# Performance work log

Measured on AMD Instinct MI355X. Metric: run time of the kernel, lower is better.

Reference implementation:

```python
import jax, jax.numpy as jnp
import numpy as np

K = 16
NUM_RBF = 32
MAX_DIST = 24.0
OUT_DIM = 256
_SPACING = MAX_DIST / (NUM_RBF - 1)
GAMMA = 1.0 / (_SPACING * _SPACING + 1e-08)
CENTERS = jnp.linspace(0.0, MAX_DIST, NUM_RBF)


def setup_inputs() -> dict:
    key = jax.random.key(0)
    k1, k2, k3 = jax.random.split(key, 3)
    B, M = 64, 1024
    # scale coords so pairwise distances span roughly [0, MAX_DIST]
    ligand_coords = jax.random.normal(k1, (B, M, 3), dtype=jnp.float32) * 8.0
    ligand_mask = jax.random.randint(k2, (B, M), 0, 2) > 0
    proj_w = jax.random.normal(k3, (OUT_DIM, K * NUM_RBF), dtype=jnp.float32) * 0.05
    return {"ligand_coords": ligand_coords, "ligand_mask": ligand_mask, "proj_w": proj_w}


def reference(ligand_coords, ligand_mask, proj_w):
    B, M, _ = ligand_coords.shape
    x = ligand_coords.astype(jnp.float32)
    # pairwise euclidean distances via the gram trick (avoids [B,M,M,3])
    sq = jnp.sum(x * x, axis=-1)                      # [B, M]
    gram = jnp.einsum('bid,bjd->bij', x, x)           # [B, M, M]
    d2 = sq[:, :, None] + sq[:, None, :] - 2.0 * gram
    dists = jnp.sqrt(jnp.maximum(d2, 1e-12))          # [B, M, M]
    eye = jnp.eye(M, dtype=bool)[None]
    valid_pair = ligand_mask[:, :, None] & ligand_mask[:, None, :]
    invalid = eye | ~valid_pair
    dists = jnp.where(invalid, jnp.inf, dists)
    # k smallest distances per atom
    neg_topk, _ = jax.lax.top_k(-dists, K)            # [B, M, K]
    topk = -neg_topk
    d_padded = jnp.where(jnp.isfinite(topk), topk, MAX_DIST)
    # RBF embed
    diff = d_padded[..., None] - CENTERS              # [B, M, K, NUM_RBF]
    rbf = jnp.exp(-GAMMA * diff * diff)
    rbf_flat = rbf.reshape(B, M, K * NUM_RBF)
    out = jnp.einsum('bmf,of->bmo', rbf_flat, proj_w)
    return out * ligand_mask[..., None].astype(out.dtype)
```

## Files before the change

kernel.cpp:

```cpp
#include <hip/hip_runtime.h>
#include <hip/hip_bf16.h>
#include <math.h>

#define MDIM 1024
#define QTOT 65536
#define KTOP 16
#define ODIM 256
#define FDIM 512

typedef float f32x4 __attribute__((ext_vector_type(4)));
typedef short s16x8 __attribute__((ext_vector_type(8)));
typedef unsigned u32x4 __attribute__((ext_vector_type(4)));

#if __has_builtin(__builtin_amdgcn_exp2f)
#define EXP2(x) __builtin_amdgcn_exp2f(x)
#else
#define EXP2(x) exp2f(x)
#endif

#define VMIN(a,b)    ({float r_; asm("v_min_f32 %0,%1,%2":"=v"(r_):"v"(a),"v"(b)); r_;})
#define VMAX(a,b)    ({float r_; asm("v_max_f32 %0,%1,%2":"=v"(r_):"v"(a),"v"(b)); r_;})

__device__ __forceinline__ int read_mask(const void* m, int i, bool is8) {
  return is8 ? (int)((const unsigned char*)m)[i] : ((const int*)m)[i];
}

__device__ __forceinline__ unsigned pack2(float lo, float hi) {
  __hip_bfloat162 h = __float22bfloat162_rn(make_float2(lo, hi));
  unsigned u;
  __builtin_memcpy(&u, &h, sizeof(u));
  return u;
}

__global__ __launch_bounds__(256) void wconv_kernel(
    const float* __restrict__ W, u32x4* __restrict__ Wb)
{
  int slot = blockIdx.x * 256 + threadIdx.x;
  int cg = slot >> 10;
  int rem = slot & 1023;
  int s = rem >> 6, l = rem & 63;
  int col = cg * 16 + (l & 15);
  int kk = s * 32 + (l >> 4) * 8;
  const float4* p = (const float4*)(W + (size_t)col * FDIM + kk);
  float4 a = p[0], b = p[1];
  u32x4 u0;
  u0[0] = pack2(a.x, a.y); u0[1] = pack2(a.z, a.w);
  u0[2] = pack2(b.x, b.y); u0[3] = pack2(b.z, b.w);
  Wb[(size_t)(cg * 16 + s) * 64 + l] = u0;
}

constexpr double SPd = 24.0 / 31.0;
constexpr double SP2d = SPd * SPd;
constexpr float ALPHA = (float)(-(SP2d / (SP2d + 1e-8)) * 1.4426950408889634);
constexpr float INV_SP = (float)(1.0 / SPd);

__device__ __forceinline__ void gen_cell(u32x4* Ab, int rf, int rowlo, int s, float d0) {
  float d = (d0 < 0.f) ? 1.0e9f : d0;
  float u = d * INV_SP;
  float C1 = (-2.0f * ALPHA) * u;
  float C0 = ALPHA * u * u;
  #pragma unroll
  for (int c8 = 0; c8 < 4; ++c8) {
    u32x4 ch;
    #pragma unroll
    for (int q = 0; q < 4; ++q) {
      const int j0 = c8 * 8 + q * 2;
      float e0 = EXP2(fmaf(C1, (float)j0,       C0) + ALPHA * (float)(j0 * j0));
      float e1 = EXP2(fmaf(C1, (float)(j0 + 1), C0) + ALPHA * (float)((j0 + 1) * (j0 + 1)));
      ch[q] = pack2(e0, e1);
    }
    Ab[rf * 1040 + s * 65 + c8 * 16 + rowlo] = ch;
  }
}

__global__ __launch_bounds__(512, 4) void fused_kernel(
    const float* __restrict__ coords, const void* __restrict__ mask,
    const u32x4* __restrict__ Wb, float* __restrict__ out)
{
  __shared__ __align__(16) char raw[66560];
  __shared__ float dvals[64][17];
  __shared__ int s_cnt;
  __shared__ int s_is8;

  float4* pts = (float4*)raw;
  short* posof = (short*)(raw + 16384);
  u32x4* Ab = (u32x4*)raw;

  const int tid = threadIdx.x;
  const int lane = tid & 63;
  const int wv = tid >> 6;
  const int bid = blockIdx.x;
  const int batch = bid >> 4;
  const int qchunk = bid & 15;

  if (tid == 0) { s_cnt = 0; s_is8 = 0; }
  __syncthreads();
  {
    unsigned w = ((const unsigned*)mask)[tid & 255];
    if (w > 1u) atomicOr(&s_is8, 1);
  }
  __syncthreads();
  const bool is8 = (s_is8 != 0);

  const float* cb = coords + (size_t)batch * MDIM * 3;
  const int mbase = batch * MDIM;

  #pragma unroll
  for (int r = 0; r < 2; ++r) {
    int a = r * 512 + tid;
    int v = read_mask(mask, mbase + a, is8);
    float x = cb[a*3+0], y = cb[a*3+1], z = cb[a*3+2];
    float S = fmaf(z, z, fmaf(y, y, x * x));
    unsigned long long bal = __ballot(v != 0);
    int base = 0;
    if (lane == 0) base = atomicAdd(&s_cnt, __popcll(bal));
    base = __shfl(base, 0);
    int pos = base + __popcll(bal & ((1ull << lane) - 1ull));
    if (v) {
      float4 p; p.x = x; p.y = y; p.z = z; p.w = S;
      pts[pos] = p;
    }
    posof[a] = (short)(v ? pos : -1);
  }
  __syncthreads();
  const int cnt = s_cnt;
  const int cntP = (cnt + 63) & ~63;
  for (int i = cnt + tid; i < cntP; i += 512) {
    float4 p; p.x = 0.f; p.y = 0.f; p.z = 0.f; p.w = 3.0e38f;
    pts[i] = p;
  }
  __syncthreads();

  const int qi = lane & 7;
  const int part = lane >> 3;
  const int qlo = wv * 8 + qi;
  const int qlocal = qchunk * 64 + qlo;
  const float qx = cb[qlocal*3+0], qy = cb[qlocal*3+1], qz = cb[qlocal*3+2];
  const float Q = fmaf(qz, qz, fmaf(qy, qy, qx * qx));
  const float m2x = -2.0f * qx, m2y = -2.0f * qy, m2z = -2.0f * qz;
  const int selfpos = posof[qlocal];
  const int lo = (cntP * part) >> 3;
  const int ng = cntP >> 6;

  float t[16];
  #pragma unroll
  for (int i = 0; i < 16; ++i) t[i] = 3.0e38f;

  for (int g = 0; g < ng; ++g) {
    const int base = lo + g * 8;
    float s[8];
    #pragma unroll
    for (int i = 0; i < 8; ++i) {
      int idx = base + ((i + part) & 7);
      float4 p = pts[idx];
      float d = fmaf(p.z, m2z, fmaf(p.y, m2y, fmaf(p.x, m2x, p.w)));
      s[i] = (idx == selfpos) ? 3.0e38f : d;
    }
    #define CES(i,j) { float mn_ = VMIN(s[i], s[j]); float mx_ = VMAX(s[i], s[j]); s[i] = mn_; s[j] = mx_; }
    CES(0,1) CES(2,3) CES(4,5) CES(6,7)
    CES(0,2) CES(1,3) CES(4,6) CES(5,7)
    CES(1,2) CES(5,6)
    CES(0,4) CES(1,5) CES(2,6) CES(3,7)
    CES(2,4) CES(3,5)
    CES(1,2) CES(3,4) CES(5,6)
    #undef CES
    #pragma unroll
    for (int i = 0; i < 8; ++i) t[8 + i] = VMIN(t[8 + i], s[7 - i]);
    #define CET(i,j) { float mn_ = VMIN(t[i], t[j]); float mx_ = VMAX(t[i], t[j]); t[i] = mn_; t[j] = mx_; }
    CET(0,8) CET(1,9) CET(2,10) CET(3,11) CET(4,12) CET(5,13) CET(6,14) CET(7,15)
    CET(0,4) CET(1,5) CET(2,6)  CET(3,7)  CET(8,12) CET(9,13) CET(10,14) CET(11,15)
    CET(0,2) CET(1,3) CET(4,6)  CET(5,7)  CET(8,10) CET(9,11) CET(12,14) CET(13,15)
    CET(0,1) CET(2,3) CET(4,5)  CET(6,7)  CET(8,9)  CET(10,11) CET(12,13) CET(14,15)
    #undef CET
  }

  #pragma unroll
  for (int stepi = 0; stepi < 3; ++stepi) {
    const int step = 8 << stepi;
    float o_[16], m[16];
    #pragma unroll
    for (int i = 0; i < 16; ++i) o_[i] = __shfl(t[i], lane ^ step);
    #pragma unroll
    for (int i = 0; i < 16; ++i) m[i] = VMIN(t[i], o_[15 - i]);
    #define CE(i,jj) { float a_ = VMIN(m[i], m[jj]); float b_ = VMAX(m[i], m[jj]); m[i] = a_; m[jj] = b_; }
    CE(0,8) CE(1,9) CE(2,10) CE(3,11) CE(4,12) CE(5,13) CE(6,14) CE(7,15)
    CE(0,4) CE(1,5) CE(2,6)  CE(3,7)  CE(8,12) CE(9,13) CE(10,14) CE(11,15)
    CE(0,2) CE(1,3) CE(4,6)  CE(5,7)  CE(8,10) CE(9,11) CE(12,14) CE(13,15)
    CE(0,1) CE(2,3) CE(4,5)  CE(6,7)  CE(8,9)  CE(10,11) CE(12,13) CE(14,15)
    #undef CE
    #pragma unroll
    for (int i = 0; i < 16; ++i) t[i] = m[i];
  }

  if (part == 0) {
    int mq = read_mask(mask, mbase + qlocal, is8);
    #pragma unroll
    for (int i = 0; i < 16; ++i) {
      float v = t[i];
      float d = (v > 1.0e37f) ? 24.0f : sqrtf(fmaxf(v + Q, 1e-12f));
      dvals[qlo][i] = mq ? d : -1.0f;
    }
  }
  __syncthreads();

  #pragma unroll
  for (int i = 0; i < 2; ++i) {
    int cellid = tid + 512 * i;
    int row = cellid >> 4, slot = cellid & 15;
    gen_cell(Ab, row >> 4, row & 15, slot, dvals[row][slot]);
  }
  __syncthreads();

  f32x4 acc[4][2];
  #pragma unroll
  for (int rf = 0; rf < 4; ++rf)
    #pragma unroll
    for (int e = 0; e < 2; ++e) acc[rf][e] = (f32x4){0.f, 0.f, 0.f, 0.f};

  u32x4 bcur[2], bnxt[2];
  #pragma unroll
  for (int e = 0; e < 2; ++e)
    bcur[e] = Wb[(size_t)((e * 8 + wv) * 16) * 64 + lane];

  #pragma unroll
  for (int s = 0; s < 16; ++s) {
    if (s < 15) {
      #pragma unroll
      for (int e = 0; e < 2; ++e)
        bnxt[e] = Wb[(size_t)((e * 8 + wv) * 16 + s + 1) * 64 + lane];
    }
    s16x8 a[4], b[2];
    #pragma unroll
    for (int rf = 0; rf < 4; ++rf) {
      u32x4 ra = Ab[rf * 1040 + s * 65 + lane];
      __builtin_memcpy(&a[rf], &ra, sizeof(ra));
    }
    #pragma unroll
    for (int e = 0; e < 2; ++e) __builtin_memcpy(&b[e], &bcur[e], sizeof(u32x4));
    #pragma unroll
    for (int rf = 0; rf < 4; ++rf)
      #pragma unroll
      for (int e = 0; e < 2; ++e)
        acc[rf][e] = __builtin_amdgcn_mfma_f32_16x16x32_bf16(a[rf], b[e], acc[rf][e], 0, 0, 0);
    #pragma unroll
    for (int e = 0; e < 2; ++e) bcur[e] = bnxt[e];
  }

  const int qbase = mbase + qchunk * 64;
  const int rb_ = (lane >> 4) * 4;
  #pragma unroll
  for (int rf = 0; rf < 4; ++rf) {
    #pragma unroll
    for (int e = 0; e < 2; ++e) {
      const int col = (e * 8 + wv) * 16 + (lane & 15);
      #pragma unroll
      for (int r = 0; r < 4; ++r)
        out[(size_t)(qbase + rf * 16 + rb_ + r) * ODIM + col] = acc[rf][e][r];
    }
  }
}

extern "C" void kernel_launch(void* const* d_in, const int* in_sizes, int n_in,
                              void* d_out, int out_size, void* d_ws, size_t ws_size,
                              hipStream_t stream) {
  const float* coords = (const float*)d_in[0];
  const void* mask = d_in[1];
  const float* W = (const float*)d_in[2];
  float* out = (float*)d_out;
  u32x4* Wb = (u32x4*)d_ws;

  hipLaunchKernelGGL(wconv_kernel, dim3(64), dim3(256), 0, stream, W, Wb);
  hipLaunchKernelGGL(fused_kernel, dim3(QTOT / 64), dim3(512), 0, stream,
                     coords, mask, Wb, out);
}
```

Before: 54.94 us.

## Keep per-lane top-8 with exact fallback when a partition exceeds eight neighbours

Each lane now keeps only its 8 smallest distances instead of 16. That halves the register list and the per-group merge network (8-wide clean instead of 16-wide). The lane partials are merged into a top-16 across the 8 partition lanes, and a wave ballot checks whether any lane's 8th value is below the merged 16th. Only in that case is the full 16-per-lane scan rerun, so the result stays exact. Point access becomes a strided interleave (pts + part, stride 8), and exp2 is emitted through inline v_exp_f32 asm. The cost is a possible second full pass whenever a single partition holds more than 8 of a query's top-16, plus an extra branch.

```diff
diff --git a/kernel.cpp b/kernel.cpp
--- a/kernel.cpp
+++ b/kernel.cpp
@@ -12,14 +12,9 @@
 typedef short s16x8 __attribute__((ext_vector_type(8)));
 typedef unsigned u32x4 __attribute__((ext_vector_type(4)));
 
-#if __has_builtin(__builtin_amdgcn_exp2f)
-#define EXP2(x) __builtin_amdgcn_exp2f(x)
-#else
-#define EXP2(x) exp2f(x)
-#endif
-
-#define VMIN(a,b)    ({float r_; asm("v_min_f32 %0,%1,%2":"=v"(r_):"v"(a),"v"(b)); r_;})
-#define VMAX(a,b)    ({float r_; asm("v_max_f32 %0,%1,%2":"=v"(r_):"v"(a),"v"(b)); r_;})
+#define VMIN(a,b)  ({float r_; asm("v_min_f32 %0,%1,%2":"=v"(r_):"v"(a),"v"(b)); r_;})
+#define VMAX(a,b)  ({float r_; asm("v_max_f32 %0,%1,%2":"=v"(r_):"v"(a),"v"(b)); r_;})
+#define VEXP2(x)   ({float r_; asm("v_exp_f32 %0,%1":"=v"(r_):"v"(x)); r_;})
 
 __device__ __forceinline__ int read_mask(const void* m, int i, bool is8) {
   return is8 ? (int)((const unsigned char*)m)[i] : ((const int*)m)[i];
@@ -31,6 +26,24 @@
   __builtin_memcpy(&u, &h, sizeof(u));
   return u;
 }
+
+#define CEx(A,i,j) { float mn_ = VMIN(A[i], A[j]); float mx_ = VMAX(A[i], A[j]); A[i] = mn_; A[j] = mx_; }
+#define SORT8(A) \
+  CEx(A,0,1) CEx(A,2,3) CEx(A,4,5) CEx(A,6,7) \
+  CEx(A,0,2) CEx(A,1,3) CEx(A,4,6) CEx(A,5,7) \
+  CEx(A,1,2) CEx(A,5,6) \
+  CEx(A,0,4) CEx(A,1,5) CEx(A,2,6) CEx(A,3,7) \
+  CEx(A,2,4) CEx(A,3,5) \
+  CEx(A,1,2) CEx(A,3,4) CEx(A,5,6)
+#define CLEAN8(A) \
+  CEx(A,0,4) CEx(A,1,5) CEx(A,2,6) CEx(A,3,7) \
+  CEx(A,0,2) CEx(A,1,3) CEx(A,4,6) CEx(A,5,7) \
+  CEx(A,0,1) CEx(A,2,3) CEx(A,4,5) CEx(A,6,7)
+#define CLEAN16(A) \
+  CEx(A,0,8) CEx(A,1,9) CEx(A,2,10) CEx(A,3,11) CEx(A,4,12) CEx(A,5,13) CEx(A,6,14) CEx(A,7,15) \
+  CEx(A,0,4) CEx(A,1,5) CEx(A,2,6)  CEx(A,3,7)  CEx(A,8,12) CEx(A,9,13) CEx(A,10,14) CEx(A,11,15) \
+  CEx(A,0,2) CEx(A,1,3) CEx(A,4,6)  CEx(A,5,7)  CEx(A,8,10) CEx(A,9,11) CEx(A,12,14) CEx(A,13,15) \
+  CEx(A,0,1) CEx(A,2,3) CEx(A,4,5)  CEx(A,6,7)  CEx(A,8,9)  CEx(A,10,11) CEx(A,12,13) CEx(A,14,15)
 
 __global__ __launch_bounds__(256) void wconv_kernel(
     const float* __restrict__ W, u32x4* __restrict__ Wb)
@@ -65,8 +78,8 @@
     #pragma unroll
     for (int q = 0; q < 4; ++q) {
       const int j0 = c8 * 8 + q * 2;
-      float e0 = EXP2(fmaf(C1, (float)j0,       C0) + ALPHA * (float)(j0 * j0));
-      float e1 = EXP2(fmaf(C1, (float)(j0 + 1), C0) + ALPHA * (float)((j0 + 1) * (j0 + 1)));
+      float e0 = VEXP2(fmaf(C1, (float)j0,       C0) + ALPHA * (float)(j0 * j0));
+      float e1 = VEXP2(fmaf(C1, (float)(j0 + 1), C0) + ALPHA * (float)((j0 + 1) * (j0 + 1)));
       ch[q] = pack2(e0, e1);
     }
     Ab[rf * 1040 + s * 65 + c8 * 16 + rowlo] = ch;
@@ -139,57 +152,85 @@
   const float Q = fmaf(qz, qz, fmaf(qy, qy, qx * qx));
   const float m2x = -2.0f * qx, m2y = -2.0f * qy, m2z = -2.0f * qz;
   const int selfpos = posof[qlocal];
-  const int lo = (cntP * part) >> 3;
-  const int ng = cntP >> 6;
+  const int selfk = ((selfpos & 7) == part) ? (selfpos >> 3) : -1;
+  const int ngroups = cntP >> 6;
+  const float4* pbase = pts + part;
+
+  float t8[8];
+  #pragma unroll
+  for (int i = 0; i < 8; ++i) t8[i] = 3.0e38f;
+
+  for (int g = 0; g < ngroups; ++g) {
+    float s[8];
+    #pragma unroll
+    for (int i = 0; i < 8; ++i) {
+      float4 p = pbase[(size_t)(g * 8 + i) * 8];
+      float d = fmaf(p.z, m2z, fmaf(p.y, m2y, fmaf(p.x, m2x, p.w)));
+      s[i] = (g * 8 + i == selfk) ? 3.0e38f : d;
+    }
+    SORT8(s)
+    float m[8];
+    #pragma unroll
+    for (int i = 0; i < 8; ++i) m[i] = VMIN(t8[i], s[7 - i]);
+    CLEAN8(m)
+    #pragma unroll
+    for (int i = 0; i < 8; ++i) t8[i] = m[i];
+  }
+  const float bound = t8[7];
 
   float t[16];
-  #pragma unroll
-  for (int i = 0; i < 16; ++i) t[i] = 3.0e38f;
-
-  for (int g = 0; g < ng; ++g) {
-    const int base = lo + g * 8;
-    float s[8];
-    #pragma unroll
-    for (int i = 0; i < 8; ++i) {
-      int idx = base + ((i + part) & 7);
-      float4 p = pts[idx];
-      float d = fmaf(p.z, m2z, fmaf(p.y, m2y, fmaf(p.x, m2x, p.w)));
-      s[i] = (idx == selfpos) ? 3.0e38f : d;
-    }
-    #define CES(i,j) { float mn_ = VMIN(s[i], s[j]); float mx_ = VMAX(s[i], s[j]); s[i] = mn_; s[j] = mx_; }
-    CES(0,1) CES(2,3) CES(4,5) CES(6,7)
-    CES(0,2) CES(1,3) CES(4,6) CES(5,7)
-    CES(1,2) CES(5,6)
-    CES(0,4) CES(1,5) CES(2,6) CES(3,7)
-    CES(2,4) CES(3,5)
-    CES(1,2) CES(3,4) CES(5,6)
-    #undef CES
-    #pragma unroll
-    for (int i = 0; i < 8; ++i) t[8 + i] = VMIN(t[8 + i], s[7 - i]);
-    #define CET(i,j) { float mn_ = VMIN(t[i], t[j]); float mx_ = VMAX(t[i], t[j]); t[i] = mn_; t[j] = mx_; }
-    CET(0,8) CET(1,9) CET(2,10) CET(3,11) CET(4,12) CET(5,13) CET(6,14) CET(7,15)
-    CET(0,4) CET(1,5) CET(2,6)  CET(3,7)  CET(8,12) CET(9,13) CET(10,14) CET(11,15)
-    CET(0,2) CET(1,3) CET(4,6)  CET(5,7)  CET(8,10) CET(9,11) CET(12,14) CET(13,15)
-    CET(0,1) CET(2,3) CET(4,5)  CET(6,7)  CET(8,9)  CET(10,11) CET(12,13) CET(14,15)
-    #undef CET
-  }
-
-  #pragma unroll
-  for (int stepi = 0; stepi < 3; ++stepi) {
-    const int step = 8 << stepi;
-    float o_[16], m[16];
-    #pragma unroll
-    for (int i = 0; i < 16; ++i) o_[i] = __shfl(t[i], lane ^ step);
-    #pragma unroll
-    for (int i = 0; i < 16; ++i) m[i] = VMIN(t[i], o_[15 - i]);
-    #define CE(i,jj) { float a_ = VMIN(m[i], m[jj]); float b_ = VMAX(m[i], m[jj]); m[i] = a_; m[jj] = b_; }
-    CE(0,8) CE(1,9) CE(2,10) CE(3,11) CE(4,12) CE(5,13) CE(6,14) CE(7,15)
-    CE(0,4) CE(1,5) CE(2,6)  CE(3,7)  CE(8,12) CE(9,13) CE(10,14) CE(11,15)
-    CE(0,2) CE(1,3) CE(4,6)  CE(5,7)  CE(8,10) CE(9,11) CE(12,14) CE(13,15)
-    CE(0,1) CE(2,3) CE(4,5)  CE(6,7)  CE(8,9)  CE(10,11) CE(12,13) CE(14,15)
-    #undef CE
+  {
+    float o[8], L[8], H[8];
+    #pragma unroll
+    for (int i = 0; i < 8; ++i) o[i] = __shfl(t8[i], lane ^ 8);
+    #pragma unroll
+    for (int i = 0; i < 8; ++i) { L[i] = VMIN(t8[i], o[7 - i]); H[i] = VMAX(t8[i], o[7 - i]); }
+    CLEAN8(L)
+    CLEAN8(H)
+    #pragma unroll
+    for (int i = 0; i < 8; ++i) { t[i] = L[i]; t[8 + i] = H[i]; }
+  }
+  #pragma unroll
+  for (int stepi = 0; stepi < 2; ++stepi) {
+    const int step = 16 << stepi;
+    float o[16], m[16];
+    #pragma unroll
+    for (int i = 0; i < 16; ++i) o[i] = __shfl(t[i], lane ^ step);
+    #pragma unroll
+    for (int i = 0; i < 16; ++i) m[i] = VMIN(t[i], o[15 - i]);
+    CLEAN16(m)
     #pragma unroll
     for (int i = 0; i < 16; ++i) t[i] = m[i];
+  }
+
+  if (__ballot(bound < t[15]) != 0ull) {
+    #pragma unroll
+    for (int i = 0; i < 16; ++i) t[i] = 3.0e38f;
+    for (int g = 0; g < ngroups; ++g) {
+      float s[8];
+      #pragma unroll
+      for (int i = 0; i < 8; ++i) {
+        float4 p = pbase[(size_t)(g * 8 + i) * 8];
+        float d = fmaf(p.z, m2z, fmaf(p.y, m2y, fmaf(p.x, m2x, p.w)));
+        s[i] = (g * 8 + i == selfk) ? 3.0e38f : d;
+      }
+      SORT8(s)
+      #pragma unroll
+      for (int i = 0; i < 8; ++i) t[8 + i] = VMIN(t[8 + i], s[7 - i]);
+      CLEAN16(t)
+    }
+    #pragma unroll
+    for (int stepi = 0; stepi < 3; ++stepi) {
+      const int step = 8 << stepi;
+      float o[16], m[16];
+      #pragma unroll
+      for (int i = 0; i < 16; ++i) o[i] = __shfl(t[i], lane ^ step);
+      #pragma unroll
+      for (int i = 0; i < 16; ++i) m[i] = VMIN(t[i], o[15 - i]);
+      CLEAN16(m)
+      #pragma unroll
+      for (int i = 0; i < 16; ++i) t[i] = m[i];
+    }
   }
 
   if (part == 0) {
```

Result: faster. 53.67 us (-2.3%).
